# Performance work log

Measured on AMD Instinct MI355X. Metric: run time of the kernel, lower is better.

The kernel has to match this reference:

```python
import jax, jax.numpy as jnp
import numpy as np

B, S, D, H = 2, 2048, 1024, 16
DK = D // H

def setup_inputs() -> dict:
    key = jax.random.key(0)
    ks = jax.random.split(key, 5)
    scale = 1.0 / np.sqrt(D)
    return {
        "x": jax.random.normal(ks[0], (B, S, D), dtype=jnp.float32),
        "W_qkv": jax.random.uniform(ks[1], (D, 3 * D), dtype=jnp.float32, minval=-scale, maxval=scale),
        "b_qkv": jax.random.uniform(ks[2], (3 * D,), dtype=jnp.float32, minval=-scale, maxval=scale),
        "W_o": jax.random.uniform(ks[3], (D, D), dtype=jnp.float32, minval=-scale, maxval=scale),
        "b_o": jax.random.uniform(ks[4], (D,), dtype=jnp.float32, minval=-scale, maxval=scale),
    }

def reference(x, W_qkv, b_qkv, W_o, b_o):
    # fused QKV projection: [B,S,3D] -> [B,S,H,3*dk]
    qkv = (x @ W_qkv + b_qkv).reshape(B, S, H, 3 * DK)
    q, k, v = qkv[..., :DK], qkv[..., DK:2 * DK], qkv[..., 2 * DK:]
    # scores [B,H,S,S]; note: original module's masked_fill is a discarded no-op, so no mask applied
    a = jnp.einsum("bqhd,bkhd->bhqk", q, k) / np.sqrt(DK).astype(np.float32)
    a = jax.nn.softmax(a, axis=-1)
    o = jnp.einsum("bhqk,bkhd->bqhd", a, v).reshape(B, S, D)
    return o @ W_o + b_o
```

## Files before the change

kernel.cpp:

```cpp
#include <hip/hip_runtime.h>
#include <hip/hip_bf16.h>

typedef __bf16 bf16;
typedef __attribute__((ext_vector_type(8))) __bf16 bf16x8;
typedef __attribute__((ext_vector_type(4))) __bf16 bf16x4;
typedef __attribute__((ext_vector_type(4))) float f32x4;
typedef __attribute__((ext_vector_type(16))) float f32x16;
typedef __attribute__((ext_vector_type(4))) unsigned int u32x4;
typedef __attribute__((ext_vector_type(2))) unsigned int u32x2;

#define DEV static __device__ __forceinline__

DEV f32x4 mfma16(bf16x8 a, bf16x8 b, f32x4 c) {
  return __builtin_amdgcn_mfma_f32_16x16x32_bf16(a, b, c, 0, 0, 0);
}
DEV f32x16 mfma32(bf16x8 a, bf16x8 b, f32x16 c) {
  return __builtin_amdgcn_mfma_f32_32x32x16_bf16(a, b, c, 0, 0, 0);
}
DEV unsigned int pk2(float a, float b) {
  unsigned short ua = __builtin_bit_cast(unsigned short, (bf16)a);
  unsigned short ub = __builtin_bit_cast(unsigned short, (bf16)b);
  return ((unsigned int)ub << 16) | ua;
}
DEV void gload16(const void* g, void* l) {
  __builtin_amdgcn_global_load_lds(
      (const __attribute__((address_space(1))) unsigned int*)g,
      (__attribute__((address_space(3))) unsigned int*)l, 16, 0, 0);
}
DEV u32x2 xhalf(unsigned int a, unsigned int b, int hi) {
#if __has_builtin(__builtin_amdgcn_permlane32_swap)
  return __builtin_amdgcn_permlane32_swap(a, b, false, false);
#else
  unsigned int xa = __shfl_xor(a, 32), xb = __shfl_xor(b, 32);
  u32x2 r;
  r.x = hi ? xb : a;
  r.y = hi ? b : xa;
  return r;
#endif
}


__global__ __launch_bounds__(256) void prep_k(
    const float* __restrict__ x, bf16* __restrict__ xb,
    const float* __restrict__ wqkv, bf16* __restrict__ wqkvT,
    const float* __restrict__ wo, bf16* __restrict__ woT) {
  __shared__ bf16 ts[64][68];
  const int tid = threadIdx.x;
  const int bid = blockIdx.x;
  if (bid < 2048) {
    int gid = bid * 256 + tid;
    const float* src = x + (size_t)gid * 8;
    f32x4 a0 = *(const f32x4*)src;
    f32x4 a1 = *(const f32x4*)(src + 4);
    bf16x8 pk;
#pragma unroll
    for (int j = 0; j < 4; ++j) { pk[j] = (bf16)a0[j]; pk[j + 4] = (bf16)a1[j]; }
    *(bf16x8*)(xb + (size_t)gid * 8) = pk;
    return;
  }
  const float* w;
  bf16* wt;
  int N, K, n0, k0;
  if (bid < 2816) {
    int r = bid - 2048;
    w = wqkv; wt = wqkvT; N = 3072; K = 1024;
    n0 = (r % 48) * 64; k0 = (r / 48) * 64;
  } else {
    int r = bid - 2816;
    w = wo; wt = woT; N = 1024; K = 1024;
    n0 = (r % 16) * 64; k0 = (r / 16) * 64;
  }
  const int tr = tid >> 4;
  const int tc = (tid & 15) * 4;
#pragma unroll
  for (int p = 0; p < 4; ++p) {
    int kr = p * 16 + tr;
    f32x4 v = *(const f32x4*)(w + (size_t)(k0 + kr) * N + n0 + tc);
#pragma unroll
    for (int j = 0; j < 4; ++j) ts[tc + j][kr] = (bf16)v[j];
  }
  __syncthreads();
#pragma unroll
  for (int p = 0; p < 4; ++p) {
    int nr = p * 16 + tr;
    bf16x4 o4;
#pragma unroll
    for (int j = 0; j < 4; ++j) o4[j] = ts[nr][tc + j];
    *(bf16x4*)(wt + (size_t)(n0 + nr) * K + k0 + tc) = o4;
  }
}

__global__ __launch_bounds__(256, 2) void qkv_gemm_k(
    const bf16* __restrict__ xb, const bf16* __restrict__ wt,
    const float* __restrict__ bias,
    bf16* __restrict__ qo, bf16* __restrict__ ko, bf16* __restrict__ vt) {
  __shared__ __align__(16) char As[16384];
  __shared__ __align__(16) char Bs[16384];
  const int tid = threadIdx.x;
  const int lane = tid & 63;
  const int wid = tid >> 6;
  const int wm = wid >> 1, wn = wid & 1;
  const int l16 = lane & 15, lhi = lane >> 4;
  const int m0 = blockIdx.y * 128;
  const int n0 = blockIdx.x * 128;
  const char* ap = (const char*)xb;
  const char* bp = (const char*)wt;

  f32x4 acc[4][4] = {};

  for (int kt = 0; kt < 1024; kt += 64) {
#pragma unroll
    for (int i = 0; i < 4; ++i) {
      int n = i * 256 + wid * 64 + lane;
      int row = n >> 3, c16 = n & 7;
      gload16(ap + (size_t)(m0 + row) * 2048 + kt * 2 + ((c16 * 16) ^ ((row & 7) << 4)),
              As + (i * 256 + wid * 64) * 16);
    }
#pragma unroll
    for (int i = 0; i < 4; ++i) {
      int n = i * 256 + wid * 64 + lane;
      int row = n >> 3, c16 = n & 7;
      gload16(bp + (size_t)(n0 + row) * 2048 + kt * 2 + ((c16 * 16) ^ ((row & 7) << 4)),
              Bs + (i * 256 + wid * 64) * 16);
    }
    __syncthreads();
#pragma unroll
    for (int kc = 0; kc < 2; ++kc) {
      bf16x8 af[4], bfr[4];
#pragma unroll
      for (int ii = 0; ii < 4; ++ii) {
        int row = wm * 64 + ii * 16 + l16;
        af[ii] = *(const bf16x8*)(As + row * 128 +
                                  ((kc * 64 + lhi * 16) ^ ((row & 7) << 4)));
      }
#pragma unroll
      for (int jj = 0; jj < 4; ++jj) {
        int n = wn * 64 + jj * 16 + l16;
        bfr[jj] = *(const bf16x8*)(Bs + n * 128 +
                                   ((kc * 64 + lhi * 16) ^ ((n & 7) << 4)));
      }
#pragma unroll
      for (int ii = 0; ii < 4; ++ii)
#pragma unroll
        for (int jj = 0; jj < 4; ++jj)
          acc[ii][jj] = mfma16(af[ii], bfr[jj], acc[ii][jj]);
    }
    __syncthreads();
  }

  const float SCQ = 0.18033688011112042f;
#pragma unroll
  for (int jj = 0; jj < 4; ++jj) {
    int nbase = n0 + wn * 64 + jj * 16;
    int h = nbase / 192;
    int rem = nbase - h * 192;
    int type = rem >> 6;
    int dk0 = rem & 63;
    float bv = bias[nbase + l16];
    if (type < 2) {
      bf16* dst = (type == 0) ? qo : ko;
      float scl = (type == 0) ? SCQ : 1.0f;
#pragma unroll
      for (int ii = 0; ii < 4; ++ii) {
#pragma unroll
        for (int r = 0; r < 4; ++r) {
          int mrow = m0 + wm * 64 + ii * 16 + lhi * 4 + r;
          int b = mrow >> 11, s = mrow & 2047;
          dst[(size_t)((b * 16 + h) * 2048 + s) * 64 + dk0 + l16] =
              (bf16)((acc[ii][jj][r] + bv) * scl);
        }
      }
    } else {
#pragma unroll
      for (int ii = 0; ii < 4; ++ii) {
        int s0 = m0 + wm * 64 + ii * 16 + lhi * 4;
        int b = s0 >> 11, s = s0 & 2047;
        bf16x4 w4;
#pragma unroll
        for (int r = 0; r < 4; ++r) w4[r] = (bf16)(acc[ii][jj][r] + bv);
        *(bf16x4*)(vt + (size_t)((b * 16 + h) * 64 + dk0 + l16) * 2048 + s) = w4;
      }
    }
  }
}

__global__ __launch_bounds__(256, 2) void attn_k(
    const bf16* __restrict__ q, const bf16* __restrict__ k,
    const bf16* __restrict__ vt, float* __restrict__ opart,
    float* __restrict__ lpart) {
  __shared__ __align__(16) char Ks[2][8192];
  __shared__ __align__(16) char Vs[2][8192];
  const int tid = threadIdx.x;
  const int lane = tid & 63;
  const int wid = tid >> 6;
  const int l31 = lane & 31;
  const int hi = lane >> 5;
  const int bh = blockIdx.x;
  const int half = blockIdx.z;
  const bf16* qp = q + (size_t)bh * 2048 * 64;
  const char* kp = (const char*)(k + (size_t)bh * 2048 * 64);
  const char* vp = (const char*)(vt + (size_t)bh * 64 * 2048);
  const int q0 = blockIdx.y * 256 + wid * 64;
  const int kv0 = half * 1024;

  bf16x8 qf0[4], qf1[4];
#pragma unroll
  for (int c = 0; c < 4; ++c) {
    qf0[c] = *(const bf16x8*)(qp + (size_t)(q0 + l31) * 64 + c * 16 + 8 * hi);
    qf1[c] = *(const bf16x8*)(qp + (size_t)(q0 + 32 + l31) * 64 + c * 16 + 8 * hi);
  }

  f32x16 ot00 = {}, ot01 = {}, ot10 = {}, ot11 = {};
  float l0 = 0.f, l1 = 0.f;

  auto STAGE = [&](int kt, int bs) {
#pragma unroll
    for (int i = 0; i < 2; ++i) {
      int n = i * 256 + wid * 64 + lane;
      int row = n >> 3, c16 = n & 7;
      const char* src = kp + (size_t)(kt + row) * 128 + ((c16 * 16) ^ ((row & 7) << 4));
      gload16(src, Ks[bs] + (i * 256 + wid * 64) * 16);
    }
#pragma unroll
    for (int i = 0; i < 2; ++i) {
      int n = i * 256 + wid * 64 + lane;
      int row = n >> 3, c16 = n & 7;
      const char* src = vp + (size_t)row * 4096 + (size_t)kt * 2 +
                        ((c16 * 16) ^ ((row & 7) << 4));
      gload16(src, Vs[bs] + (i * 256 + wid * 64) * 16);
    }
  };

  STAGE(kv0, 0);
  __syncthreads();

  for (int t = 0; t < 16; ++t) {
    int bs = t & 1;
    if (t < 15) STAGE(kv0 + (t + 1) * 64, bs ^ 1);

#pragma unroll
    for (int kb = 0; kb < 2; ++kb) {
      bf16x8 kf[4];
#pragma unroll
      for (int c = 0; c < 4; ++c) {
        int row = kb * 32 + l31;
        kf[c] = *(const bf16x8*)(Ks[bs] + row * 128 +
                                 ((c * 32 + 16 * hi) ^ ((row & 7) << 4)));
      }
      f32x16 st0 = {}, st1 = {};
      __builtin_amdgcn_s_setprio(1);
#pragma unroll
      for (int c = 0; c < 4; ++c) {
        st0 = mfma32(kf[c], qf0[c], st0);
        st1 = mfma32(kf[c], qf1[c], st1);
      }
      __builtin_amdgcn_s_setprio(0);
      float p0[16], p1[16];
#pragma unroll
      for (int r = 0; r < 16; ++r) {
        p0[r] = __builtin_amdgcn_exp2f(st0[r]);
        l0 += p0[r];
        p1[r] = __builtin_amdgcn_exp2f(st1[r]);
        l1 += p1[r];
      }

#pragma unroll
      for (int c2 = 0; c2 < 2; ++c2) {
        const int off = c2 * 8;
        unsigned int a0 = pk2(p0[off + 0], p0[off + 1]);
        unsigned int a1 = pk2(p0[off + 2], p0[off + 3]);
        unsigned int a2 = pk2(p0[off + 4], p0[off + 5]);
        unsigned int a3 = pk2(p0[off + 6], p0[off + 7]);
        u32x2 s02 = xhalf(a0, a2, hi);
        u32x2 s13 = xhalf(a1, a3, hi);
        u32x4 wwa;
        wwa.x = s02.x; wwa.y = s13.x; wwa.z = s02.y; wwa.w = s13.y;
        bf16x8 pb0 = __builtin_bit_cast(bf16x8, wwa);
        unsigned int b0 = pk2(p1[off + 0], p1[off + 1]);
        unsigned int b1 = pk2(p1[off + 2], p1[off + 3]);
        unsigned int b2 = pk2(p1[off + 4], p1[off + 5]);
        unsigned int b3 = pk2(p1[off + 6], p1[off + 7]);
        u32x2 t02 = xhalf(b0, b2, hi);
        u32x2 t13 = xhalf(b1, b3, hi);
        u32x4 wwb;
        wwb.x = t02.x; wwb.y = t13.x; wwb.z = t02.y; wwb.w = t13.y;
        bf16x8 pb1 = __builtin_bit_cast(bf16x8, wwb);

        int col = kb * 64 + c2 * 32 + 16 * hi;
        int r0 = l31, r1 = 32 + l31;
        bf16x8 vf0 = *(const bf16x8*)(Vs[bs] + r0 * 128 + (col ^ ((r0 & 7) << 4)));
        bf16x8 vf1 = *(const bf16x8*)(Vs[bs] + r1 * 128 + (col ^ ((r1 & 7) << 4)));
        __builtin_amdgcn_s_setprio(1);
        ot00 = mfma32(vf0, pb0, ot00);
        ot01 = mfma32(vf1, pb0, ot01);
        ot10 = mfma32(vf0, pb1, ot10);
        ot11 = mfma32(vf1, pb1, ot11);
        __builtin_amdgcn_s_setprio(0);
      }
    }
    __syncthreads();
  }

  float lt0 = l0 + __shfl_xor(l0, 32);
  float lt1 = l1 + __shfl_xor(l1, 32);
  if (hi == 0) {
    lpart[(size_t)(half * 32 + bh) * 2048 + q0 + l31] = lt0;
    lpart[(size_t)(half * 32 + bh) * 2048 + q0 + 32 + l31] = lt1;
  }

  float* op0 = opart + ((size_t)(half * 32 + bh) * 2048 + q0 + l31) * 64;
  float* op1 = opart + ((size_t)(half * 32 + bh) * 2048 + q0 + 32 + l31) * 64;
#pragma unroll
  for (int g = 0; g < 4; ++g) {
    f32x4 a4, b4, c4, d4;
#pragma unroll
    for (int j = 0; j < 4; ++j) {
      a4[j] = ot00[g * 4 + j];
      b4[j] = ot01[g * 4 + j];
      c4[j] = ot10[g * 4 + j];
      d4[j] = ot11[g * 4 + j];
    }
    *(f32x4*)(op0 + 8 * g + 4 * hi) = a4;
    *(f32x4*)(op0 + 32 + 8 * g + 4 * hi) = b4;
    *(f32x4*)(op1 + 8 * g + 4 * hi) = c4;
    *(f32x4*)(op1 + 32 + 8 * g + 4 * hi) = d4;
  }
}

__global__ __launch_bounds__(256) void comb_k(const float* __restrict__ opart,
                                              const float* __restrict__ lpart,
                                              bf16* __restrict__ o) {
  const size_t HS = 32ull * 2048 * 64;
  int gid = blockIdx.x * 256 + threadIdx.x;
  int dq = gid & 15;
  int s = (gid >> 4) & 2047;
  int bh = gid >> 15;
  size_t i0 = ((size_t)bh * 2048 + s) * 64 + dq * 4;
  f32x4 a = *(const f32x4*)(opart + i0);
  f32x4 b2 = *(const f32x4*)(opart + HS + i0);
  float l0 = lpart[(size_t)bh * 2048 + s];
  float l1 = lpart[32ull * 2048 + (size_t)bh * 2048 + s];
  float inv = 1.f / (l0 + l1);
  int b = bh >> 4, h = bh & 15;
  bf16x4 r;
#pragma unroll
  for (int j = 0; j < 4; ++j) r[j] = (bf16)((a[j] + b2[j]) * inv);
  *(bf16x4*)(o + (size_t)(b * 2048 + s) * 1024 + h * 64 + dq * 4) = r;
}

__global__ __launch_bounds__(256, 2) void out_gemm_k(
    const bf16* __restrict__ a, const bf16* __restrict__ wt,
    const float* __restrict__ bias, float* __restrict__ out) {
  __shared__ __align__(16) char As[16384];
  __shared__ __align__(16) char Bs[16384];
  const int tid = threadIdx.x;
  const int lane = tid & 63;
  const int wid = tid >> 6;
  const int wm = wid >> 1, wn = wid & 1;
  const int l16 = lane & 15, lhi = lane >> 4;
  const int m0 = blockIdx.y * 128;
  const int n0 = blockIdx.x * 128;
  const char* ap = (const char*)a;
  const char* bp = (const char*)wt;

  f32x4 acc[4][4] = {};

  for (int kt = 0; kt < 1024; kt += 64) {
#pragma unroll
    for (int i = 0; i < 4; ++i) {
      int n = i * 256 + wid * 64 + lane;
      int row = n >> 3, c16 = n & 7;
      gload16(ap + (size_t)(m0 + row) * 2048 + kt * 2 + ((c16 * 16) ^ ((row & 7) << 4)),
              As + (i * 256 + wid * 64) * 16);
    }
#pragma unroll
    for (int i = 0; i < 4; ++i) {
      int n = i * 256 + wid * 64 + lane;
      int row = n >> 3, c16 = n & 7;
      gload16(bp + (size_t)(n0 + row) * 2048 + kt * 2 + ((c16 * 16) ^ ((row & 7) << 4)),
              Bs + (i * 256 + wid * 64) * 16);
    }
    __syncthreads();
#pragma unroll
    for (int kc = 0; kc < 2; ++kc) {
      bf16x8 af[4], bfr[4];
#pragma unroll
      for (int ii = 0; ii < 4; ++ii) {
        int row = wm * 64 + ii * 16 + l16;
        af[ii] = *(const bf16x8*)(As + row * 128 +
                                  ((kc * 64 + lhi * 16) ^ ((row & 7) << 4)));
      }
#pragma unroll
      for (int jj = 0; jj < 4; ++jj) {
        int n = wn * 64 + jj * 16 + l16;
        bfr[jj] = *(const bf16x8*)(Bs + n * 128 +
                                   ((kc * 64 + lhi * 16) ^ ((n & 7) << 4)));
      }
#pragma unroll
      for (int ii = 0; ii < 4; ++ii)
#pragma unroll
        for (int jj = 0; jj < 4; ++jj)
          acc[ii][jj] = mfma16(af[ii], bfr[jj], acc[ii][jj]);
    }
    __syncthreads();
  }

#pragma unroll
  for (int jj = 0; jj < 4; ++jj) {
    int nbase = n0 + wn * 64 + jj * 16;
    float bv = bias[nbase + l16];
#pragma unroll
    for (int ii = 0; ii < 4; ++ii) {
#pragma unroll
      for (int r = 0; r < 4; ++r) {
        int mrow = m0 + wm * 64 + ii * 16 + lhi * 4 + r;
        out[(size_t)mrow * 1024 + nbase + l16] = acc[ii][jj][r] + bv;
      }
    }
  }
}

extern "C" void kernel_launch(void* const* d_in, const int* in_sizes, int n_in,
                              void* d_out, int out_size, void* d_ws, size_t ws_size,
                              hipStream_t stream) {
  const float* x = (const float*)d_in[0];
  const float* wqkv = (const float*)d_in[1];
  const float* bqkv = (const float*)d_in[2];
  const float* wo = (const float*)d_in[3];
  const float* bo = (const float*)d_in[4];
  float* out = (float*)d_out;

  bf16* qws = (bf16*)d_ws;
  bf16* kws = qws + 4194304;
  bf16* vtws = kws + 4194304;
  bf16* ows = vtws + 4194304;
  bf16* wqkvT = ows + 4194304;
  bf16* woT = wqkvT + 3145728;
  float* opart = (float*)(woT + 1048576);
  float* lpart = opart + 8388608;
  bf16* xbf = (bf16*)opart;

  prep_k<<<3072, 256, 0, stream>>>(x, xbf, wqkv, wqkvT, wo, woT);
  qkv_gemm_k<<<dim3(24, 32), 256, 0, stream>>>(xbf, wqkvT, bqkv, qws, kws, vtws);
  attn_k<<<dim3(32, 8, 2), 256, 0, stream>>>(qws, kws, vtws, opart, lpart);
  comb_k<<<4096, 256, 0, stream>>>(opart, lpart, ows);
  out_gemm_k<<<dim3(8, 32), 256, 0, stream>>>(ows, woT, bo, out);
}
```

Baseline: 127.7 us.

## Split attention KV range four ways with bf16 partial outputs

The attention kernel now splits the key/value sequence into four chunks of 512 instead of two of 1024, launching twice as many blocks, and raises the launch-bounds occupancy hint to 4. Partial outputs are stored as bf16 instead of fp32 to halve the write traffic, and the combine kernel sums four partials. The aim is better CU occupancy and less partial-buffer bandwidth. The trade-offs are more combine work, extra bf16 rounding of unnormalized partial sums, and possible register pressure from the higher occupancy target. The softmax apparently has no running-max rescaling, so partials combine by plain summation.

```diff
diff --git a/kernel.cpp b/kernel.cpp
--- a/kernel.cpp
+++ b/kernel.cpp
@@ -184,9 +184,9 @@
   }
 }
 
-__global__ __launch_bounds__(256, 2) void attn_k(
+__global__ __launch_bounds__(256, 4) void attn_k(
     const bf16* __restrict__ q, const bf16* __restrict__ k,
-    const bf16* __restrict__ vt, float* __restrict__ opart,
+    const bf16* __restrict__ vt, bf16* __restrict__ opart,
     float* __restrict__ lpart) {
   __shared__ __align__(16) char Ks[2][8192];
   __shared__ __align__(16) char Vs[2][8192];
@@ -201,7 +201,7 @@
   const char* kp = (const char*)(k + (size_t)bh * 2048 * 64);
   const char* vp = (const char*)(vt + (size_t)bh * 64 * 2048);
   const int q0 = blockIdx.y * 256 + wid * 64;
-  const int kv0 = half * 1024;
+  const int kv0 = half * 512;
 
   bf16x8 qf0[4], qf1[4];
 #pragma unroll
@@ -234,9 +234,9 @@
   STAGE(kv0, 0);
   __syncthreads();
 
-  for (int t = 0; t < 16; ++t) {
+  for (int t = 0; t < 8; ++t) {
     int bs = t & 1;
-    if (t < 15) STAGE(kv0 + (t + 1) * 64, bs ^ 1);
+    if (t < 7) STAGE(kv0 + (t + 1) * 64, bs ^ 1);
 
 #pragma unroll
     for (int kb = 0; kb < 2; ++kb) {
@@ -308,26 +308,26 @@
     lpart[(size_t)(half * 32 + bh) * 2048 + q0 + 32 + l31] = lt1;
   }
 
-  float* op0 = opart + ((size_t)(half * 32 + bh) * 2048 + q0 + l31) * 64;
-  float* op1 = opart + ((size_t)(half * 32 + bh) * 2048 + q0 + 32 + l31) * 64;
+  bf16* op0 = opart + ((size_t)(half * 32 + bh) * 2048 + q0 + l31) * 64;
+  bf16* op1 = opart + ((size_t)(half * 32 + bh) * 2048 + q0 + 32 + l31) * 64;
 #pragma unroll
   for (int g = 0; g < 4; ++g) {
-    f32x4 a4, b4, c4, d4;
+    bf16x4 a4, b4, c4, d4;
 #pragma unroll
     for (int j = 0; j < 4; ++j) {
-      a4[j] = ot00[g * 4 + j];
-      b4[j] = ot01[g * 4 + j];
-      c4[j] = ot10[g * 4 + j];
-      d4[j] = ot11[g * 4 + j];
-    }
-    *(f32x4*)(op0 + 8 * g + 4 * hi) = a4;
-    *(f32x4*)(op0 + 32 + 8 * g + 4 * hi) = b4;
-    *(f32x4*)(op1 + 8 * g + 4 * hi) = c4;
-    *(f32x4*)(op1 + 32 + 8 * g + 4 * hi) = d4;
-  }
-}
-
-__global__ __launch_bounds__(256) void comb_k(const float* __restrict__ opart,
+      a4[j] = (bf16)ot00[g * 4 + j];
+      b4[j] = (bf16)ot01[g * 4 + j];
+      c4[j] = (bf16)ot10[g * 4 + j];
+      d4[j] = (bf16)ot11[g * 4 + j];
+    }
+    *(bf16x4*)(op0 + 8 * g + 4 * hi) = a4;
+    *(bf16x4*)(op0 + 32 + 8 * g + 4 * hi) = b4;
+    *(bf16x4*)(op1 + 8 * g + 4 * hi) = c4;
+    *(bf16x4*)(op1 + 32 + 8 * g + 4 * hi) = d4;
+  }
+}
+
+__global__ __launch_bounds__(256) void comb_k(const bf16* __restrict__ opart,
                                               const float* __restrict__ lpart,
                                               bf16* __restrict__ o) {
   const size_t HS = 32ull * 2048 * 64;
@@ -336,15 +336,21 @@
   int s = (gid >> 4) & 2047;
   int bh = gid >> 15;
   size_t i0 = ((size_t)bh * 2048 + s) * 64 + dq * 4;
-  f32x4 a = *(const f32x4*)(opart + i0);
-  f32x4 b2 = *(const f32x4*)(opart + HS + i0);
-  float l0 = lpart[(size_t)bh * 2048 + s];
-  float l1 = lpart[32ull * 2048 + (size_t)bh * 2048 + s];
-  float inv = 1.f / (l0 + l1);
+  float l = 0.f;
+#pragma unroll
+  for (int sp = 0; sp < 4; ++sp) l += lpart[(size_t)(sp * 32 + bh) * 2048 + s];
+  f32x4 acc = {};
+#pragma unroll
+  for (int sp = 0; sp < 4; ++sp) {
+    bf16x4 v = *(const bf16x4*)(opart + sp * HS + i0);
+#pragma unroll
+    for (int j = 0; j < 4; ++j) acc[j] += (float)v[j];
+  }
+  float inv = 1.f / l;
   int b = bh >> 4, h = bh & 15;
   bf16x4 r;
 #pragma unroll
-  for (int j = 0; j < 4; ++j) r[j] = (bf16)((a[j] + b2[j]) * inv);
+  for (int j = 0; j < 4; ++j) r[j] = (bf16)(acc[j] * inv);
   *(bf16x4*)(o + (size_t)(b * 2048 + s) * 1024 + h * 64 + dq * 4) = r;
 }
 
@@ -436,13 +442,13 @@
   bf16* ows = vtws + 4194304;
   bf16* wqkvT = ows + 4194304;
   bf16* woT = wqkvT + 3145728;
-  float* opart = (float*)(woT + 1048576);
-  float* lpart = opart + 8388608;
-  bf16* xbf = (bf16*)opart;
+  bf16* opart = woT + 1048576;
+  float* lpart = (float*)(opart + 16777216);
+  bf16* xbf = opart;
 
   prep_k<<<3072, 256, 0, stream>>>(x, xbf, wqkv, wqkvT, wo, woT);
   qkv_gemm_k<<<dim3(24, 32), 256, 0, stream>>>(xbf, wqkvT, bqkv, qws, kws, vtws);
-  attn_k<<<dim3(32, 8, 2), 256, 0, stream>>>(qws, kws, vtws, opart, lpart);
+  attn_k<<<dim3(32, 8, 4), 256, 0, stream>>>(qws, kws, vtws, opart, lpart);
   comb_k<<<4096, 256, 0, stream>>>(opart, lpart, ows);
   out_gemm_k<<<dim3(8, 32), 256, 0, stream>>>(ows, woT, bo, out);
 }
```

Result: slower. 359.3 us (+181.4%).
